# Optimization experiments

Hardware: AMD Instinct MI355X
Metric: run time of the kernel (lower is better)

## Reference

```python
import jax, jax.numpy as jnp
import numpy as np

IN_C, OUT_C = 32, 64
KSIZE = (3, 3, 3)


def setup_inputs() -> dict:
    key = jax.random.key(0)
    k1, k2 = jax.random.split(key)
    x = jax.random.normal(k1, (2, IN_C, 64, 64, 64), dtype=jnp.float32)
    # One learnable scalar per (out_channel, in_channel, kz, ky, kx) basis function.
    W = jax.random.normal(k2, (OUT_C, IN_C) + KSIZE, dtype=jnp.float32) * 0.05
    return {"x": x, "W": W}


def reference(x, W):
    # Original: for each (oc, ic, kz, ky, kx), out[:, oc] += basis(x[:, ic, shifted_slices])
    # With scalar-weight bases this is exactly a VALID (unpadded) 3D convolution:
    # out[b, o, d, h, w] = sum_{i, kz, ky, kx} W[o, i, kz, ky, kx] * x[b, i, d+kz, h+ky, w+kx]
    return jax.lax.conv_general_dilated(
        x, W,
        window_strides=(1, 1, 1),
        padding="VALID",
        dimension_numbers=("NCDHW", "OIDHW", "NCDHW"),
    )
```

## Files before the change

kernel.cpp:

```cpp
#include <hip/hip_runtime.h>
#include <hip/hip_bf16.h>

#define DIN 64
#define DOUT 62
#define ICH 32
#define OCH 64

typedef __bf16 bf16x8 __attribute__((ext_vector_type(8)));
typedef float f32x4 __attribute__((ext_vector_type(4)));
typedef float f32x8 __attribute__((ext_vector_type(8)));
typedef float f32x16 __attribute__((ext_vector_type(16)));

#define AS1U(p) ((const __attribute__((address_space(1))) unsigned int*)(p))
#define AS3U(p) ((__attribute__((address_space(3))) unsigned int*)(p))

__global__ void prep_w(const float* __restrict__ W, unsigned short* __restrict__ Wre3) {
    int idx = blockIdx.x * 256 + threadIdx.x;
    if (idx >= 27 * OCH * ICH) return;
    int j    = idx & 7;
    int lane = (idx >> 3) & 63;
    int kh   = (idx >> 9) & 1;
    int mt   = (idx >> 10) & 1;
    int tap  = idx >> 11;
    int oc   = mt * 32 + (lane & 31);
    int ic   = kh * 16 + (lane >> 5) * 8 + j;
    float v  = W[((size_t)oc * ICH + ic) * 27 + tap];
    Wre3[idx] = __builtin_bit_cast(unsigned short, (__bf16)v);
}

__global__ void prep_x(const float* __restrict__ x, unsigned short* __restrict__ xp) {
    int idx = blockIdx.x * 256 + threadIdx.x;
    int w = idx & 63;
    int s = (idx >> 6) & 3;
    int y = (idx >> 8) & 63;
    int z = (idx >> 14) & 63;
    int b = idx >> 20;
    const float* xb = x + ((size_t)(b * ICH + s * 8)) * 262144 + (size_t)z * 4096 + y * 64 + w;
    bf16x8 pk;
#pragma unroll
    for (int j = 0; j < 8; ++j)
        pk[j] = (__bf16)xb[(size_t)j * 262144];
    ((int4*)xp)[idx] = __builtin_bit_cast(int4, pk);
}

__global__ __launch_bounds__(256, 3) void conv3d_mfma_pk(
    const unsigned short* __restrict__ Wre3,
    const unsigned short* __restrict__ xp,
    float* __restrict__ out)
{
    __shared__ char xs[2 * 24576 + 256];

    const int tid  = threadIdx.x;
    const int lane = tid & 63;
    const int wave = tid >> 6;

    const int orig = blockIdx.x;
    const int lid  = (orig & 7) * 248 + (orig >> 3);
    const int ht = lid & 15;
    const int rr = lid >> 4;
    const int d  = rr % DOUT;
    const int b  = rr / DOUT;
    const int h0 = ht * 4;

    const int l31 = lane & 31;
    const int lhi = lane >> 5;
    const int row = wave;

    auto stage_chunk = [&](char* buf, int z, int i) {
        int c  = wave * 6 + i;
        int yl = c >> 2;
        int sl = c & 3;
        int srow = h0 + yl; if (srow > 63) srow = 63;
        const unsigned short* src =
            xp + ((((size_t)(b * DIN + z) * DIN + srow) * 4 + sl) * 64) * 8 + lane * 8;
        __builtin_amdgcn_global_load_lds(AS1U(src), AS3U(buf + c * 1024), 16, 0, 0);
    };
    auto loadA = [&](int tap, int4* af) {
        const int4* wp = (const int4*)Wre3 + (size_t)tap * 256 + lane;
#pragma unroll
        for (int q = 0; q < 4; ++q)
            af[q] = wp[q * 64];
    };
    auto readB = [&](const char* buf, int ky, int kx, int4* dst) {
#pragma unroll
        for (int kh = 0; kh < 2; ++kh) {
            const int g = kh * 2 + lhi;
#pragma unroll
            for (int nt = 0; nt < 2; ++nt) {
                int wb = nt * 32 + l31 + kx;
                if (wb > 63) wb = 63;
                dst[kh * 2 + nt] = *(const int4*)(buf + (((row + ky) * 4 + g) * 64 + wb) * 16);
            }
        }
    };

    char* bufA = xs;
    char* bufB = xs + 24576;

#pragma unroll
    for (int i = 0; i < 6; ++i) stage_chunk(bufA, d, i);
    int4 af[2][4];
    loadA(0, af[0]);

    f32x16 acc[2][2];
#pragma unroll
    for (int mt = 0; mt < 2; ++mt)
#pragma unroll
        for (int nt = 0; nt < 2; ++nt)
#pragma unroll
            for (int r = 0; r < 16; ++r) acc[mt][nt][r] = 0.f;

    __syncthreads();

    int4 bfr[2][4];

#pragma unroll
    for (int kz = 0; kz < 3; ++kz) {
        char* cur = (kz & 1) ? bufB : bufA;
        char* nxt = (kz & 1) ? bufA : bufB;
        readB(cur, 0, 0, bfr[0]);

#pragma unroll
        for (int t = 0; t < 9; ++t) {
            const int T = kz * 9 + t;
            if (T < 26) loadA(T + 1, af[(T + 1) & 1]);
            if (t < 8)  readB(cur, (t + 1) / 3, (t + 1) % 3, bfr[(t + 1) & 1]);
            if (kz < 2 && t < 6) stage_chunk(nxt, d + kz + 1, t);

            __builtin_amdgcn_s_setprio(1);
#pragma unroll
            for (int mt = 0; mt < 2; ++mt)
#pragma unroll
                for (int nt = 0; nt < 2; ++nt) {
                    acc[mt][nt] = __builtin_amdgcn_mfma_f32_32x32x16_bf16(
                        __builtin_bit_cast(bf16x8, af[T & 1][mt * 2 + 0]),
                        __builtin_bit_cast(bf16x8, bfr[t & 1][0 * 2 + nt]),
                        acc[mt][nt], 0, 0, 0);
                    acc[mt][nt] = __builtin_amdgcn_mfma_f32_32x32x16_bf16(
                        __builtin_bit_cast(bf16x8, af[T & 1][mt * 2 + 1]),
                        __builtin_bit_cast(bf16x8, bfr[t & 1][1 * 2 + nt]),
                        acc[mt][nt], 0, 0, 0);
                }
            __builtin_amdgcn_s_setprio(0);
        }
        if (kz < 2) __syncthreads();
    }

    const int h = h0 + row;
    if (h < DOUT) {
#pragma unroll
        for (int mt = 0; mt < 2; ++mt) {
#pragma unroll
            for (int r = 0; r < 16; ++r) {
                int oc = mt * 32 + (r & 3) + 8 * (r >> 2) + 4 * lhi;
                size_t ob = ((((size_t)b * OCH + oc) * DOUT + d) * DOUT + h) * DOUT;
#pragma unroll
                for (int nt = 0; nt < 2; ++nt) {
                    int ww = nt * 32 + l31;
                    if (ww < DOUT) out[ob + ww] = acc[mt][nt][r];
                }
            }
        }
    }
}

__global__ __launch_bounds__(256, 3) void conv3d_mfma_fb(
    const float* __restrict__ x, const float* __restrict__ W,
    float* __restrict__ out)
{
    __shared__ char xs[2][6 * 66 * 64];

    const int tid  = threadIdx.x;
    const int lane = tid & 63;
    const int wave = tid >> 6;

    const int orig = blockIdx.x;
    const int lid  = (orig & 7) * 248 + (orig >> 3);
    const int ht = lid & 15;
    const int rr = lid >> 4;
    const int d  = rr % DOUT;
    const int b  = rr / DOUT;
    const int h0 = ht * 4;

    const int wlo = lane & 15;
    const int whi = lane >> 4;
    const int row = wave;

    const int icg  = wave;
    const int w    = lane;
    const int slot = icg ^ ((w >> 1) & 3);

    auto issueRow = [&](int z, int y) -> f32x8 {
        int gy = h0 + y; if (gy > 63) gy = 63;
        const float* xp2 = x + (((size_t)(b * ICH + icg * 8) * DIN + z) * DIN + gy) * DIN + w;
        f32x8 s;
#pragma unroll
        for (int j = 0; j < 8; ++j) s[j] = xp2[(size_t)j * DIN * DIN * DIN];
        return s;
    };
    auto writeRow = [&](char* buf, int y, f32x8 s) {
        bf16x8 pk;
#pragma unroll
        for (int j = 0; j < 8; ++j) pk[j] = (__bf16)s[j];
        *(int4*)(buf + ((y * 66 + w) * 64 + slot * 16)) = __builtin_bit_cast(int4, pk);
    };
    auto loadA = [&](int tap, int4* af) {
#pragma unroll
        for (int mt = 0; mt < 4; ++mt) {
            const float* wp = W + ((size_t)(mt * 16 + wlo) * ICH + whi * 8) * 27 + tap;
            bf16x8 t;
#pragma unroll
            for (int j = 0; j < 8; ++j) t[j] = (__bf16)wp[j * 27];
            af[mt] = __builtin_bit_cast(int4, t);
        }
    };
    auto readB = [&](const char* buf, int ky, int kx, int4* dst) {
#pragma unroll
        for (int nt = 0; nt < 4; ++nt) {
            int wb = nt * 16 + wlo + kx;
            int sl = whi ^ ((wb >> 1) & 3);
            dst[nt] = *(const int4*)(buf + (((row + ky) * 66 + wb) * 64 + sl * 16));
        }
    };

    if (tid < 96) {
        int bu = tid / 48, q2 = tid % 48;
        int y = q2 >> 3, q = q2 & 7;
        int w2 = 64 + (q >> 2), sl = q & 3;
        *(int4*)(xs[bu] + ((y * 66 + w2) * 64 + sl * 16)) = int4{0, 0, 0, 0};
    }
    {
        f32x8 s0 = issueRow(d, 0), s1 = issueRow(d, 1), s2 = issueRow(d, 2);
        writeRow(xs[0], 0, s0); s0 = issueRow(d, 3);
        writeRow(xs[0], 1, s1); s1 = issueRow(d, 4);
        writeRow(xs[0], 2, s2); s2 = issueRow(d, 5);
        writeRow(xs[0], 3, s0); writeRow(xs[0], 4, s1); writeRow(xs[0], 5, s2);
    }
    int4 af[2][4];
    loadA(0, af[0]);
    __syncthreads();

    f32x4 acc[4][4];
#pragma unroll
    for (int mt = 0; mt < 4; ++mt)
#pragma unroll
        for (int nt = 0; nt < 4; ++nt)
            acc[mt][nt] = f32x4{0.f, 0.f, 0.f, 0.f};

    int4 bfr[2][4];

#pragma unroll
    for (int kz = 0; kz < 3; ++kz) {
        char* cur = xs[kz & 1];
        char* nxt = xs[(kz + 1) & 1];
        f32x8 s0, s1, s2;
        readB(cur, 0, 0, bfr[0]);
#pragma unroll
        for (int t = 0; t < 9; ++t) {
            const int T = kz * 9 + t;
            if (T < 26) loadA(T + 1, af[(T + 1) & 1]);
            if (t < 8)  readB(cur, (t + 1) / 3, (t + 1) % 3, bfr[(t + 1) & 1]);
            if (kz < 2) {
                if (t == 3) writeRow(nxt, 0, s0);
                if (t == 4) writeRow(nxt, 1, s1);
                if (t == 5) writeRow(nxt, 2, s2);
                if (t == 6) writeRow(nxt, 3, s0);
                if (t == 7) writeRow(nxt, 4, s1);
                if (t == 8) writeRow(nxt, 5, s2);
                if (t == 0) s0 = issueRow(d + kz + 1, 0);
                if (t == 1) s1 = issueRow(d + kz + 1, 1);
                if (t == 2) s2 = issueRow(d + kz + 1, 2);
                if (t == 3) s0 = issueRow(d + kz + 1, 3);
                if (t == 4) s1 = issueRow(d + kz + 1, 4);
                if (t == 5) s2 = issueRow(d + kz + 1, 5);
            }
#pragma unroll
            for (int mt = 0; mt < 4; ++mt)
#pragma unroll
                for (int nt = 0; nt < 4; ++nt)
                    acc[mt][nt] = __builtin_amdgcn_mfma_f32_16x16x32_bf16(
                        __builtin_bit_cast(bf16x8, af[T & 1][mt]),
                        __builtin_bit_cast(bf16x8, bfr[t & 1][nt]),
                        acc[mt][nt], 0, 0, 0);
        }
        if (kz < 2) __syncthreads();
    }

    const int h = h0 + row;
    if (h < DOUT) {
#pragma unroll
        for (int mt = 0; mt < 4; ++mt) {
#pragma unroll
            for (int r = 0; r < 4; ++r) {
                int oc = mt * 16 + whi * 4 + r;
                size_t ob = ((((size_t)b * OCH + oc) * DOUT + d) * DOUT + h) * DOUT;
#pragma unroll
                for (int nt = 0; nt < 4; ++nt) {
                    int ww = nt * 16 + wlo;
                    if (ww < DOUT) out[ob + ww] = acc[mt][nt][r];
                }
            }
        }
    }
}

extern "C" void kernel_launch(void* const* d_in, const int* in_sizes, int n_in,
                              void* d_out, int out_size, void* d_ws, size_t ws_size,
                              hipStream_t stream) {
    const float* x = (const float*)d_in[0];
    const float* W = (const float*)d_in[1];
    float* out = (float*)d_out;

    const dim3 grid(2 * DOUT * 16);
    const size_t wre_elems = (size_t)27 * OCH * ICH;
    const size_t xp_elems  = (size_t)2 * DIN * DIN * DIN * ICH;
    const size_t need = (wre_elems + xp_elems) * 2 + 256;

    if (ws_size >= need) {
        unsigned short* Wre3 = (unsigned short*)d_ws;
        unsigned short* xp   = Wre3 + wre_elems;
        prep_w<<<216, 256, 0, stream>>>(W, Wre3);
        prep_x<<<8192, 256, 0, stream>>>(x, xp);
        conv3d_mfma_pk<<<grid, 256, 0, stream>>>(Wre3, xp, out);
    } else {
        conv3d_mfma_fb<<<grid, 256, 0, stream>>>(x, W, out);
    }
}
```

Measured before the change: 88.18 us.

## Use 512-thread blocks covering 8 output rows and drop B-operand register prefetch

Each block now computes 8 output rows with 8 waves instead of 4 rows with 4 waves. It stages 10 input rows per z-slice into larger double-buffered LDS, which cuts the relative halo traffic from global memory. The B-fragment register double buffer is removed: each tap reads its B operands from LDS right before its MFMAs, with the MFMA loop reordered by k-half. This lowers register pressure, but it exposes LDS read latency and the 80KB of LDS per block limits how many blocks fit on a CU.

```diff
diff --git a/kernel.cpp b/kernel.cpp
--- a/kernel.cpp
+++ b/kernel.cpp
@@ -43,31 +43,31 @@
     ((int4*)xp)[idx] = __builtin_bit_cast(int4, pk);
 }
 
-__global__ __launch_bounds__(256, 3) void conv3d_mfma_pk(
+__global__ __launch_bounds__(512, 4) void conv3d_mfma_pk(
     const unsigned short* __restrict__ Wre3,
     const unsigned short* __restrict__ xp,
     float* __restrict__ out)
 {
-    __shared__ char xs[2 * 24576 + 256];
+    __shared__ char xs[2][40960];
 
     const int tid  = threadIdx.x;
     const int lane = tid & 63;
     const int wave = tid >> 6;
 
     const int orig = blockIdx.x;
-    const int lid  = (orig & 7) * 248 + (orig >> 3);
-    const int ht = lid & 15;
-    const int rr = lid >> 4;
+    const int lid  = (orig & 7) * 124 + (orig >> 3);
+    const int ht = lid & 7;
+    const int rr = lid >> 3;
     const int d  = rr % DOUT;
     const int b  = rr / DOUT;
-    const int h0 = ht * 4;
+    const int h0 = ht * 8;
 
     const int l31 = lane & 31;
     const int lhi = lane >> 5;
     const int row = wave;
 
     auto stage_chunk = [&](char* buf, int z, int i) {
-        int c  = wave * 6 + i;
+        int c  = wave * 5 + i;
         int yl = c >> 2;
         int sl = c & 3;
         int srow = h0 + yl; if (srow > 63) srow = 63;
@@ -94,11 +94,8 @@
         }
     };
 
-    char* bufA = xs;
-    char* bufB = xs + 24576;
-
-#pragma unroll
-    for (int i = 0; i < 6; ++i) stage_chunk(bufA, d, i);
+#pragma unroll
+    for (int i = 0; i < 5; ++i) stage_chunk(xs[0], d, i);
     int4 af[2][4];
     loadA(0, af[0]);
 
@@ -112,35 +109,30 @@
 
     __syncthreads();
 
-    int4 bfr[2][4];
-
 #pragma unroll
     for (int kz = 0; kz < 3; ++kz) {
-        char* cur = (kz & 1) ? bufB : bufA;
-        char* nxt = (kz & 1) ? bufA : bufB;
-        readB(cur, 0, 0, bfr[0]);
+        char* cur = xs[kz & 1];
+        char* nxt = xs[(kz + 1) & 1];
 
 #pragma unroll
         for (int t = 0; t < 9; ++t) {
             const int T = kz * 9 + t;
+            int4 bfr[4];
+            readB(cur, t / 3, t % 3, bfr);
             if (T < 26) loadA(T + 1, af[(T + 1) & 1]);
-            if (t < 8)  readB(cur, (t + 1) / 3, (t + 1) % 3, bfr[(t + 1) & 1]);
-            if (kz < 2 && t < 6) stage_chunk(nxt, d + kz + 1, t);
+            if (kz < 2 && t < 5) stage_chunk(nxt, d + kz + 1, t);
 
             __builtin_amdgcn_s_setprio(1);
 #pragma unroll
-            for (int mt = 0; mt < 2; ++mt)
-#pragma unroll
-                for (int nt = 0; nt < 2; ++nt) {
-                    acc[mt][nt] = __builtin_amdgcn_mfma_f32_32x32x16_bf16(
-                        __builtin_bit_cast(bf16x8, af[T & 1][mt * 2 + 0]),
-                        __builtin_bit_cast(bf16x8, bfr[t & 1][0 * 2 + nt]),
-                        acc[mt][nt], 0, 0, 0);
-                    acc[mt][nt] = __builtin_amdgcn_mfma_f32_32x32x16_bf16(
-                        __builtin_bit_cast(bf16x8, af[T & 1][mt * 2 + 1]),
-                        __builtin_bit_cast(bf16x8, bfr[t & 1][1 * 2 + nt]),
-                        acc[mt][nt], 0, 0, 0);
-                }
+            for (int kh = 0; kh < 2; ++kh)
+#pragma unroll
+                for (int mt = 0; mt < 2; ++mt)
+#pragma unroll
+                    for (int nt = 0; nt < 2; ++nt)
+                        acc[mt][nt] = __builtin_amdgcn_mfma_f32_32x32x16_bf16(
+                            __builtin_bit_cast(bf16x8, af[T & 1][mt * 2 + kh]),
+                            __builtin_bit_cast(bf16x8, bfr[kh * 2 + nt]),
+                            acc[mt][nt], 0, 0, 0);
             __builtin_amdgcn_s_setprio(0);
         }
         if (kz < 2) __syncthreads();
@@ -311,7 +303,6 @@
     const float* W = (const float*)d_in[1];
     float* out = (float*)d_out;
 
-    const dim3 grid(2 * DOUT * 16);
     const size_t wre_elems = (size_t)27 * OCH * ICH;
     const size_t xp_elems  = (size_t)2 * DIN * DIN * DIN * ICH;
     const size_t need = (wre_elems + xp_elems) * 2 + 256;
@@ -321,8 +312,8 @@
         unsigned short* xp   = Wre3 + wre_elems;
         prep_w<<<216, 256, 0, stream>>>(W, Wre3);
         prep_x<<<8192, 256, 0, stream>>>(x, xp);
-        conv3d_mfma_pk<<<grid, 256, 0, stream>>>(Wre3, xp, out);
+        conv3d_mfma_pk<<<dim3(2 * DOUT * 8), 512, 0, stream>>>(Wre3, xp, out);
     } else {
-        conv3d_mfma_fb<<<grid, 256, 0, stream>>>(x, W, out);
-    }
-}
+        conv3d_mfma_fb<<<dim3(2 * DOUT * 16), 256, 0, stream>>>(x, W, out);
+    }
+}
```

New measurement: 90.26 us. +2.4%, slower.
